# Optimization experiments

Measured on AMD Instinct MI355X. Metric: run time of the kernel, lower is better.

The kernel has to match this reference:

```python
import jax, jax.numpy as jnp
import numpy as np

N_NODES = 100000
N_EDGES = 1000000
N_QUERY = 100000
F_IN = 64
HIDDEN = 64
LABEL_DIM = 2


def setup_inputs() -> dict:
    key = jax.random.key(0)
    ks = jax.random.split(key, 16)
    inp = {}
    for i, nm in enumerate(["Xr", "Xi", "Xj", "Xk"]):
        inp[nm] = jax.random.normal(ks[i], (N_NODES, F_IN), dtype=jnp.float32)
    for i, nm in enumerate(["norm_r", "norm_i", "norm_j", "norm_k"]):
        inp[nm] = jax.random.normal(ks[4 + i], (N_EDGES,), dtype=jnp.float32) * 0.1
    inp["edge_index"] = jax.random.randint(ks[8], (2, N_EDGES), 0, N_NODES)
    inp["query_edges"] = jax.random.randint(ks[9], (N_QUERY, 2), 0, N_NODES)
    s1 = (2.0 / (F_IN + HIDDEN)) ** 0.5  # glorot
    inp["W1"] = jax.random.normal(ks[10], (4, F_IN, HIDDEN), dtype=jnp.float32) * s1
    inp["b1"] = jnp.zeros((4, HIDDEN), dtype=jnp.float32)
    s2 = (2.0 / (HIDDEN + HIDDEN)) ** 0.5
    inp["W2"] = jax.random.normal(ks[11], (4, HIDDEN, HIDDEN), dtype=jnp.float32) * s2
    inp["b2"] = jnp.zeros((4, HIDDEN), dtype=jnp.float32)
    inp["Cw"] = jax.random.normal(ks[12], (LABEL_DIM, 8 * HIDDEN), dtype=jnp.float32) * 0.05
    inp["Cb"] = jnp.zeros((LABEL_DIM,), dtype=jnp.float32)
    return inp


def _quaconv(Xs, src, dst, norms, W, b, n_nodes):
    # Xs: list of 4 [N,F] components; norms: list of 4 [E] Laplacian norms.
    # P[a][b] = propagate(X_a, -norm_b) = scatter_add over dst of (-norm_b)_e * X_a[src_e]
    P = []
    for a in range(4):
        G = Xs[a][src]  # [E, F] gather, reused for all 4 norms
        P.append([jax.ops.segment_sum((-norms[b])[:, None] * G, dst, num_segments=n_nodes)
                  for b in range(4)])
    Tr = P[0][0] - P[1][1] - P[2][2] - P[3][3]
    Ti = P[1][0] + P[0][1] + P[3][2] - P[2][3]
    Tj = P[2][0] - P[3][1] + P[0][2] + P[1][3]
    Tk = P[3][0] + P[2][1] - P[1][2] + P[0][3]
    Wr, Wi, Wj, Wk = W[0], W[1], W[2], W[3]
    out_r = Tr @ Wr - Ti @ Wi - Tj @ Wj - Tk @ Wk + b[0]
    out_i = Tr @ Wi + Ti @ Wr + Tj @ Wk - Tk @ Wj + b[1]
    out_j = Tr @ Wj - Ti @ Wk + Tj @ Wr + Tk @ Wi + b[2]
    out_k = Tr @ Wk + Ti @ Wj - Tj @ Wi + Tk @ Wr + b[3]
    return out_r, out_i, out_j, out_k


def _forward(Xr, Xi, Xj, Xk, norm_r, norm_i, norm_j, norm_k,
             W1, b1, W2, b2, Cw, Cb, edge_index, query_edges):
    src, dst = edge_index[0], edge_index[1]
    n = Xr.shape[0]
    norms = [norm_r, norm_i, norm_j, norm_k]
    Xs = [Xr, Xi, Xj, Xk]
    for W, b in ((W1, b1), (W2, b2)):
        Xs = list(_quaconv(Xs, src, dst, norms, W, b, n))
        # complex_relu_layer_different: mask = 1.0*(x>=0); mask*x == relu(x)
        Xs = [jax.nn.relu(x) for x in Xs]
    q0, q1 = query_edges[:, 0], query_edges[:, 1]
    # cat(real[q0], real[q1], imag_i[q0], imag_i[q1], ...) -> [Eq, 8*hidden]
    feats = jnp.concatenate([c[idx] for c in Xs for idx in (q0, q1)], axis=-1)
    # dropout is identity at inference; Conv1d(kernel=1) == linear over channels
    logits = feats @ Cw.T + Cb  # [Eq, label_dim]
    return jax.nn.log_softmax(logits, axis=-1)


def reference(Xr, Xi, Xj, Xk, norm_r, norm_i, norm_j, norm_k,
              W1, b1, W2, b2, Cw, Cb, edge_index, query_edges):
    return _forward(Xr, Xi, Xj, Xk, norm_r, norm_i, norm_j, norm_k,
                    W1, b1, W2, b2, Cw, Cb, edge_index, query_edges)
```

## Files before the change

kernel.cpp:

```cpp
#include <hip/hip_runtime.h>
#include <hip/hip_bf16.h>

#define N_NODESC 100000
#define N_EDGESC 1000000
#define N_QUERYC 100000

typedef short short8 __attribute__((ext_vector_type(8)));
typedef short s16x2 __attribute__((ext_vector_type(2)));
typedef float f32x4 __attribute__((ext_vector_type(4)));

__device__ __forceinline__ float ldf(const void* p, int i, int isbf) {
  return isbf ? __bfloat162float(((const __hip_bfloat16*)p)[i])
              : ((const float*)p)[i];
}
__device__ __forceinline__ unsigned short f2b(float x) {
  __hip_bfloat16 h = __float2bfloat16(x);
  return *(unsigned short*)&h;
}
__device__ __forceinline__ float b2f(unsigned int u) {
  return __uint_as_float(u << 16);
}
__device__ __forceinline__ s16x2 u2s(unsigned u) {
  union { unsigned u; s16x2 s; } c; c.u = u; return c.s;
}
__device__ __forceinline__ void gload16(const void* g, void* l) {
  __builtin_amdgcn_global_load_lds(
      (const __attribute__((address_space(1))) void*)g,
      (__attribute__((address_space(3))) void*)l, 16, 0, 0);
}

__global__ void k_sniff(const void* x, int* flag) {
  __shared__ int cnt;
  int t = threadIdx.x;
  if (t == 0) cnt = 0;
  __syncthreads();
  const unsigned short* h = (const unsigned short*)x;
  int local = 0;
  for (int i = t; i < 4096; i += 256) {
    int e = (h[i] >> 7) & 0xFF;
    if (e >= 107 && e <= 133) local++;
  }
  atomicAdd(&cnt, local);
  __syncthreads();
  if (t == 0) *flag = (cnt >= 3482) ? 1 : 0;
}

__global__ void k_hist(const int* __restrict__ dst, int* __restrict__ cnt, int ne) {
  int e = blockIdx.x * 256 + threadIdx.x;
  if (e < ne) atomicAdd(&cnt[dst[e]], 1);
}

__global__ void k_scan1(const int* __restrict__ cnt, int* __restrict__ off,
                        int* __restrict__ partials, int n) {
  __shared__ int s[1024];
  int t = threadIdx.x;
  int idx = blockIdx.x * 1024 + t;
  int v = (idx < n) ? cnt[idx] : 0;
  s[t] = v;
  __syncthreads();
  for (int d = 1; d < 1024; d <<= 1) {
    int tmp = (t >= d) ? s[t - d] : 0;
    __syncthreads();
    s[t] += tmp;
    __syncthreads();
  }
  if (idx < n) off[idx] = s[t] - v;
  if (t == 1023) partials[blockIdx.x] = s[1023];
}

__global__ void k_scan2(const int* __restrict__ partials, int* __restrict__ pref,
                        int* __restrict__ off, int nb, int npos) {
  __shared__ int s[128];
  int t = threadIdx.x;
  int v = (t < nb) ? partials[t] : 0;
  s[t] = v;
  __syncthreads();
  for (int d = 1; d < 128; d <<= 1) {
    int tmp = (t >= d) ? s[t - d] : 0;
    __syncthreads();
    s[t] += tmp;
    __syncthreads();
  }
  if (t < nb) pref[t] = s[t] - v;
  if (t == 127) off[npos] = s[127];
}

__global__ void k_scan3(int* __restrict__ off, const int* __restrict__ pref,
                        int* __restrict__ cursor, int n) {
  int i = blockIdx.x * 256 + threadIdx.x;
  if (i < n) {
    int o = off[i] + pref[i >> 10];
    off[i] = o;
    cursor[i] = o;
  }
}

__global__ void k_fill(const int* __restrict__ ei,
                       const void* nr, const void* ni, const void* nj, const void* nk,
                       const int* __restrict__ flagp, int* __restrict__ cursor,
                       uint4* __restrict__ recs, int ne) {
  int isbf = *flagp;
  int e = blockIdx.x * 256 + threadIdx.x;
  if (e >= ne) return;
  int s = ei[e];
  int d = ei[ne + e];
  int pos = atomicAdd(&cursor[d], 1);
  uint4 r;
  r.x = (unsigned)s;
  r.y = (unsigned)f2b(-ldf(nr, e, isbf)) | ((unsigned)f2b(-ldf(ni, e, isbf)) << 16);
  r.z = (unsigned)f2b(-ldf(nj, e, isbf)) | ((unsigned)f2b(-ldf(nk, e, isbf)) << 16);
  r.w = 0;
  recs[pos] = r;
}

__global__ __launch_bounds__(256) void k_ilv(
    const void* X0, const void* X1, const void* X2, const void* X3,
    const int* __restrict__ flagp, unsigned short* __restrict__ Xg, int n) {
  int isbf = *flagp;
  int lane = threadIdx.x & 63;
  int node = blockIdx.x * 4 + (threadIdx.x >> 6);
  if (node >= n) return;
  int idx = node * 64 + lane;
  unsigned int lo = f2b(ldf(X0, idx, isbf)) | ((unsigned int)f2b(ldf(X1, idx, isbf)) << 16);
  unsigned int hi = f2b(ldf(X2, idx, isbf)) | ((unsigned int)f2b(ldf(X3, idx, isbf)) << 16);
  uint2 g = make_uint2(lo, hi);
  *(uint2*)(Xg + (size_t)node * 256 + lane * 4) = g;
}

#if __has_builtin(__builtin_amdgcn_fdot2_f32_bf16)
#define USE_DOT2 1
#else
#define USE_DOT2 0
#endif
__global__ __launch_bounds__(256, 8) void k_agg(
    const unsigned short* __restrict__ Xg, const int* __restrict__ off,
    const uint4* __restrict__ recs, unsigned short* __restrict__ Tf, int nnodes) {
  __shared__ unsigned short tl[4][256];
  int lane = threadIdx.x & 63;
  int w = threadIdx.x >> 6;
  int node = __builtin_amdgcn_readfirstlane(blockIdx.x * 4 + w);
  if (node >= nnodes) return;
  int rs = off[node], re = off[node + 1];
  float tr = 0.f, ti = 0.f, tj = 0.f, tk = 0.f;

  auto qacc = [&](uint2 g, unsigned mx, unsigned my) {
#if USE_DOT2
    unsigned a = mx, b = my;
    unsigned sa = (a >> 16) | (a << 16);
    unsigned sb = (b >> 16) | (b << 16);
    unsigned A1 = a ^ 0x80000000u;
    unsigned A2 = b ^ 0x80008000u;
    unsigned B2 = sb ^ 0x00008000u;
    unsigned D2 = sb ^ 0x80000000u;
    s16x2 gx = u2s(g.x), gy = u2s(g.y);
    tr = __builtin_amdgcn_fdot2_f32_bf16(u2s(A1), gx, tr, false);
    tr = __builtin_amdgcn_fdot2_f32_bf16(u2s(A2), gy, tr, false);
    ti = __builtin_amdgcn_fdot2_f32_bf16(u2s(sa), gx, ti, false);
    ti = __builtin_amdgcn_fdot2_f32_bf16(u2s(B2), gy, ti, false);
    tj = __builtin_amdgcn_fdot2_f32_bf16(u2s(b),  gx, tj, false);
    tj = __builtin_amdgcn_fdot2_f32_bf16(u2s(A1), gy, tj, false);
    tk = __builtin_amdgcn_fdot2_f32_bf16(u2s(D2), gx, tk, false);
    tk = __builtin_amdgcn_fdot2_f32_bf16(u2s(sa), gy, tk, false);
#else
    float mr = __uint_as_float(mx << 16), mi = __uint_as_float(mx & 0xffff0000u);
    float mj = __uint_as_float(my << 16), mk = __uint_as_float(my & 0xffff0000u);
    float xr = __uint_as_float(g.x << 16), xi = __uint_as_float(g.x & 0xffff0000u);
    float xj = __uint_as_float(g.y << 16), xk = __uint_as_float(g.y & 0xffff0000u);
    tr += mr * xr - mi * xi - mj * xj - mk * xk;
    ti += mr * xi + mi * xr + mj * xk - mk * xj;
    tj += mr * xj - mi * xk + mj * xr + mk * xi;
    tk += mr * xk + mi * xj - mj * xi + mk * xr;
#endif
  };

  int e = rs;
  for (; e + 8 <= re; e += 8) {
    int ss[8];
    unsigned sx[8], sy[8];
#pragma unroll
    for (int u = 0; u < 8; u++) {
      uint4 r = recs[e + u];
      ss[u] = __builtin_amdgcn_readfirstlane((int)r.x);
      sx[u] = __builtin_amdgcn_readfirstlane(r.y);
      sy[u] = __builtin_amdgcn_readfirstlane(r.z);
    }
    uint2 g[8];
#pragma unroll
    for (int u = 0; u < 8; u++)
      g[u] = *(const uint2*)(Xg + (size_t)ss[u] * 256 + lane * 4);
#pragma unroll
    for (int u = 0; u < 8; u++) qacc(g[u], sx[u], sy[u]);
  }
  for (; e < re; ++e) {
    uint4 r = recs[e];
    int s = __builtin_amdgcn_readfirstlane((int)r.x);
    unsigned mx = __builtin_amdgcn_readfirstlane(r.y);
    unsigned my = __builtin_amdgcn_readfirstlane(r.z);
    uint2 g0 = *(const uint2*)(Xg + (size_t)s * 256 + lane * 4);
    qacc(g0, mx, my);
  }

  tl[w][lane] = f2b(tr);
  tl[w][64 + lane] = f2b(ti);
  tl[w][128 + lane] = f2b(tj);
  tl[w][192 + lane] = f2b(tk);
  __builtin_amdgcn_wave_barrier();
  if (lane < 32) {
    uint4 v = *(const uint4*)&tl[w][lane * 8];
    size_t o = (size_t)(node >> 4) * 4096 + (lane >> 2) * 512 + (lane & 3) * 128 +
               (node & 15) * 8;
    *(uint4*)(Tf + o) = v;
  }
}

__global__ void k_weff(const void* W, const void* b, const int* __restrict__ flagp,
                       unsigned short* __restrict__ Wq, float* __restrict__ bcat) {
  int isbf = *flagp;
  int t = blockIdx.x * 256 + threadIdx.x;
  int w4 = t >> 12;
  int h = (t >> 6) & 63;
  int kk = t & 63;
  int s = (kk >> 3) ^ (h & 7);
  Wq[(w4 * 64 + h) * 64 + s * 8 + (kk & 7)] = f2b(ldf(W, w4 * 4096 + kk * 64 + h, isbf));
  if (t < 256) bcat[t] = ldf(b, t, isbf);
}

__global__ __launch_bounds__(256, 2) void k_gemm(
    const unsigned short* __restrict__ A, const unsigned short* __restrict__ Wq,
    const float* __restrict__ bias, int M, int mode,
    unsigned short* __restrict__ XgOut,
    float* __restrict__ P, const void* Cw, const int* __restrict__ flagp) {
  __shared__ unsigned short Wsm[16384];

  int t = threadIdx.x;
  int lane = t & 63;
  int w = t >> 6;
  int l15 = lane & 15, quad = lane >> 4;
  int m0 = blockIdx.x * 64;
  int hh = (w & 1) * 32;

#pragma unroll
  for (int i = 0; i < 8; i++)
    gload16((const char*)Wq + (size_t)(i * 256 + t) * 16,
            (char*)Wsm + (size_t)(i * 256 + w * 64) * 16);
  __syncthreads();

  short8 av[2][8];
  int n16 = blockIdx.x * 4 + (w >> 1) * 2;
#pragma unroll
  for (int mi = 0; mi < 2; mi++)
#pragma unroll
    for (int kc = 0; kc < 8; kc++)
      av[mi][kc] = *(const short8*)(A + (size_t)(n16 + mi) * 4096 + kc * 512 + lane * 8);

  f32x4 acc[2][4][2];
#pragma unroll
  for (int mi = 0; mi < 2; mi++)
#pragma unroll
    for (int c = 0; c < 4; c++)
#pragma unroll
      for (int hb = 0; hb < 2; hb++) acc[mi][c][hb] = (f32x4){0.f, 0.f, 0.f, 0.f};

#pragma unroll
  for (int kc = 0; kc < 8; kc++) {
    int a = kc >> 1;
    short8 bv[4][2];
#pragma unroll
    for (int c = 0; c < 4; c++) {
      int w4 = a ^ c;
      int neg = (0x3950 >> (a * 4 + c)) & 1;
#pragma unroll
      for (int hb = 0; hb < 2; hb++) {
        int h = hh + hb * 16 + l15;
        int lc = ((kc & 1) * 4 + quad) ^ (l15 & 7);
        short8 bb = *(const short8*)&Wsm[(w4 * 64 + h) * 64 + lc * 8];
        if (neg) {
          uint4 u = *(uint4*)&bb;
          u.x ^= 0x80008000u; u.y ^= 0x80008000u;
          u.z ^= 0x80008000u; u.w ^= 0x80008000u;
          bb = *(short8*)&u;
        }
        bv[c][hb] = bb;
      }
    }
#pragma unroll
    for (int mi = 0; mi < 2; mi++)
#pragma unroll
      for (int c = 0; c < 4; c++)
#pragma unroll
        for (int hb = 0; hb < 2; hb++)
          acc[mi][c][hb] =
              __builtin_amdgcn_mfma_f32_16x16x32_bf16(av[mi][kc], bv[c][hb], acc[mi][c][hb], 0, 0, 0);
  }

  float bias_v[4][2];
#pragma unroll
  for (int c = 0; c < 4; c++)
#pragma unroll
    for (int hb = 0; hb < 2; hb++) bias_v[c][hb] = bias[c * 64 + hh + hb * 16 + l15];

  if (mode == 0) {
#pragma unroll
    for (int mi = 0; mi < 2; mi++) {
#pragma unroll
      for (int hb = 0; hb < 2; hb++) {
#pragma unroll
        for (int r = 0; r < 4; r++) {
          int node = m0 + (w >> 1) * 32 + mi * 16 + quad * 4 + r;
          unsigned int lo =
              f2b(fmaxf(acc[mi][0][hb][r] + bias_v[0][hb], 0.f)) |
              ((unsigned int)f2b(fmaxf(acc[mi][1][hb][r] + bias_v[1][hb], 0.f)) << 16);
          unsigned int hi =
              f2b(fmaxf(acc[mi][2][hb][r] + bias_v[2][hb], 0.f)) |
              ((unsigned int)f2b(fmaxf(acc[mi][3][hb][r] + bias_v[3][hb], 0.f)) << 16);
          *(uint2*)(XgOut + (size_t)node * 256 + (hh + hb * 16 + l15) * 4) =
              make_uint2(lo, hi);
        }
      }
    }
  } else {
    int isbf = *flagp;
    float cw[4][2][4];
#pragma unroll
    for (int c = 0; c < 4; c++)
#pragma unroll
      for (int hb = 0; hb < 2; hb++) {
        int h = hh + hb * 16 + l15;
#pragma unroll
        for (int d = 0; d < 2; d++)
#pragma unroll
          for (int e = 0; e < 2; e++)
            cw[c][hb][e + 2 * d] = ldf(Cw, d * 512 + c * 128 + e * 64 + h, isbf);
      }
#pragma unroll
    for (int mi = 0; mi < 2; mi++) {
#pragma unroll
      for (int r = 0; r < 4; r++) {
        int node = m0 + (w >> 1) * 32 + mi * 16 + quad * 4 + r;
        float pd0 = 0.f, pd1 = 0.f, pd2 = 0.f, pd3 = 0.f;
#pragma unroll
        for (int c = 0; c < 4; c++)
#pragma unroll
          for (int hb = 0; hb < 2; hb++) {
            float v = fmaxf(acc[mi][c][hb][r] + bias_v[c][hb], 0.f);
            pd0 += v * cw[c][hb][0];
            pd1 += v * cw[c][hb][1];
            pd2 += v * cw[c][hb][2];
            pd3 += v * cw[c][hb][3];
          }
#pragma unroll
        for (int o = 1; o < 16; o <<= 1) {
          pd0 += __shfl_xor(pd0, o);
          pd1 += __shfl_xor(pd1, o);
          pd2 += __shfl_xor(pd2, o);
          pd3 += __shfl_xor(pd3, o);
        }
        if (l15 == 0 && node < M) {
          atomicAdd(&P[node * 4 + 0], pd0);
          atomicAdd(&P[node * 4 + 1], pd1);
          atomicAdd(&P[node * 4 + 2], pd2);
          atomicAdd(&P[node * 4 + 3], pd3);
        }
      }
    }
  }
}

__global__ void k_query(const int* __restrict__ qe, const float* __restrict__ P,
                        const void* Cb, const int* __restrict__ flagp,
                        void* out, int nq) {
  int isbf = *flagp;
  int q = blockIdx.x * 256 + threadIdx.x;
  if (q >= nq) return;
  int q0 = qe[q * 2], q1 = qe[q * 2 + 1];
  float l0 = P[q0 * 4 + 0] + P[q1 * 4 + 1] + ldf(Cb, 0, isbf);
  float l1 = P[q0 * 4 + 2] + P[q1 * 4 + 3] + ldf(Cb, 1, isbf);
  float m = fmaxf(l0, l1);
  float lse = m + logf(expf(l0 - m) + expf(l1 - m));
  float o0 = l0 - lse, o1 = l1 - lse;
  if (isbf) {
    __hip_bfloat16* o = (__hip_bfloat16*)out;
    o[q * 2] = __float2bfloat16(o0);
    o[q * 2 + 1] = __float2bfloat16(o1);
  } else {
    float* o = (float*)out;
    o[q * 2] = o0;
    o[q * 2 + 1] = o1;
  }
}

extern "C" void kernel_launch(void* const* d_in, const int* in_sizes, int n_in,
                              void* d_out, int out_size, void* d_ws, size_t ws_size,
                              hipStream_t stream) {
  const int N = N_NODESC, NE = N_EDGESC, NQ = N_QUERYC;
  const int NPAD = 100224;

  char* w = (char*)d_ws;
  auto alloc = [&](size_t bytes) -> void* {
    void* p = (void*)w;
    w += (bytes + 255) & ~(size_t)255;
    return p;
  };
  int* flag       = (int*)alloc(4);
  int* offsets    = (int*)alloc((size_t)(N + 1) * 4);
  int* cursor     = (int*)alloc((size_t)N * 4);
  int* partials   = (int*)alloc(128 * 4);
  int* pref       = (int*)alloc(128 * 4);
  uint4* recs     = (uint4*)alloc((size_t)NE * 16);
  unsigned short* Tf = (unsigned short*)alloc((size_t)NPAD * 256 * 2);
  unsigned short* Xg = (unsigned short*)alloc((size_t)NPAD * 256 * 2);
  unsigned short* Wq = (unsigned short*)alloc(16384 * 2);
  float* bcat     = (float*)alloc(256 * 4);
  float* P        = (float*)alloc((size_t)N * 4 * 4);
  (void)ws_size; (void)n_in; (void)in_sizes; (void)out_size;

  const int* ei = (const int*)d_in[8];

  k_sniff<<<1, 256, 0, stream>>>(d_in[0], flag);

  hipMemsetAsync(cursor, 0, (size_t)N * 4, stream);
  hipMemsetAsync(P, 0, (size_t)N * 16, stream);
  k_hist<<<(NE + 255) / 256, 256, 0, stream>>>(ei + NE, cursor, NE);
  k_scan1<<<(N + 1023) / 1024, 1024, 0, stream>>>(cursor, offsets, partials, N);
  k_scan2<<<1, 128, 0, stream>>>(partials, pref, offsets, (N + 1023) / 1024, N);
  k_scan3<<<(N + 255) / 256, 256, 0, stream>>>(offsets, pref, cursor, N);
  k_fill<<<(NE + 255) / 256, 256, 0, stream>>>(ei, d_in[4], d_in[5], d_in[6], d_in[7],
                                               flag, cursor, recs, NE);

  k_ilv<<<(N + 3) / 4, 256, 0, stream>>>(d_in[0], d_in[1], d_in[2], d_in[3], flag, Xg, N);

  int ggrid = (N + 63) / 64;

  k_agg<<<(N + 3) / 4, 256, 0, stream>>>(Xg, offsets, recs, Tf, N);
  k_weff<<<64, 256, 0, stream>>>(d_in[10], d_in[11], flag, Wq, bcat);
  k_gemm<<<ggrid, 256, 0, stream>>>(Tf, Wq, bcat, N, 0, Xg, nullptr, nullptr, flag);

  k_agg<<<(N + 3) / 4, 256, 0, stream>>>(Xg, offsets, recs, Tf, N);
  k_weff<<<64, 256, 0, stream>>>(d_in[12], d_in[13], flag, Wq, bcat);
  k_gemm<<<ggrid, 256, 0, stream>>>(Tf, Wq, bcat, N, 1, nullptr, P, d_in[14], flag);

  k_query<<<(NQ + 255) / 256, 256, 0, stream>>>((const int*)d_in[9], P, d_in[15],
                                                flag, d_out, NQ);
}
```

Measured before the change: 553.5 us.

## Balance aggregation by edges per wave with software-pipelined record and gather loads

Result: slower. 613.0 us (+10.8%).

```diff
diff --git a/kernel.cpp b/kernel.cpp
--- a/kernel.cpp
+++ b/kernel.cpp
@@ -4,6 +4,7 @@
 #define N_NODESC 100000
 #define N_EDGESC 1000000
 #define N_QUERYC 100000
+#define AGG_WAVES 8192
 
 typedef short short8 __attribute__((ext_vector_type(8)));
 typedef short s16x2 __attribute__((ext_vector_type(2)));
@@ -93,6 +94,20 @@
     off[i] = o;
     cursor[i] = o;
   }
+}
+
+__global__ void k_bounds(const int* __restrict__ off, int* __restrict__ bound,
+                         int nnodes, int nedges, int nwaves) {
+  int gw = blockIdx.x * 256 + threadIdx.x;
+  if (gw > nwaves) return;
+  if (gw == nwaves) { bound[gw] = nnodes; return; }
+  long long target = (long long)gw * nedges / nwaves;
+  int lo = 0, hi = nnodes;
+  while (lo < hi) {
+    int mid = (lo + hi) >> 1;
+    if ((long long)off[mid] >= target) hi = mid; else lo = mid + 1;
+  }
+  bound[gw] = lo;
 }
 
 __global__ void k_fill(const int* __restrict__ ei,
@@ -132,16 +147,43 @@
 #else
 #define USE_DOT2 0
 #endif
-__global__ __launch_bounds__(256, 8) void k_agg(
+__global__ __launch_bounds__(256, 4) void k_agg(
     const unsigned short* __restrict__ Xg, const int* __restrict__ off,
-    const uint4* __restrict__ recs, unsigned short* __restrict__ Tf, int nnodes) {
+    const uint4* __restrict__ recs, unsigned short* __restrict__ Tf,
+    const int* __restrict__ bound, int nnodes, int nwaves) {
   __shared__ unsigned short tl[4][256];
   int lane = threadIdx.x & 63;
   int w = threadIdx.x >> 6;
-  int node = __builtin_amdgcn_readfirstlane(blockIdx.x * 4 + w);
-  if (node >= nnodes) return;
-  int rs = off[node], re = off[node + 1];
+  int gw = blockIdx.x * 4 + w;
+  if (gw >= nwaves) return;
+
+  int ns  = __builtin_amdgcn_readfirstlane(bound[gw]);
+  int ne_ = __builtin_amdgcn_readfirstlane(bound[gw + 1]);
+  if (ns >= ne_) return;
+  int es = __builtin_amdgcn_readfirstlane(off[ns]);
+  int ee = __builtin_amdgcn_readfirstlane(off[ne_]);
+
+  int nw_ = ns;
+  int rend_e = __builtin_amdgcn_readfirstlane(off[nw_ + 1]);
   float tr = 0.f, ti = 0.f, tj = 0.f, tk = 0.f;
+
+  auto flush = [&]() {
+    tl[w][lane] = f2b(tr);
+    tl[w][64 + lane] = f2b(ti);
+    tl[w][128 + lane] = f2b(tj);
+    tl[w][192 + lane] = f2b(tk);
+    __builtin_amdgcn_wave_barrier();
+    if (lane < 32) {
+      uint4 v = *(const uint4*)&tl[w][lane * 8];
+      size_t o = (size_t)(nw_ >> 4) * 4096 + (lane >> 2) * 512 + (lane & 3) * 128 +
+                 (nw_ & 15) * 8;
+      *(uint4*)(Tf + o) = v;
+    }
+    __builtin_amdgcn_wave_barrier();
+    tr = ti = tj = tk = 0.f;
+    nw_++;
+    if (nw_ < ne_) rend_e = __builtin_amdgcn_readfirstlane(off[nw_ + 1]);
+  };
 
   auto qacc = [&](uint2 g, unsigned mx, unsigned my) {
 #if USE_DOT2
@@ -173,44 +215,97 @@
 #endif
   };
 
-  int e = rs;
-  for (; e + 8 <= re; e += 8) {
-    int ss[8];
-    unsigned sx[8], sy[8];
-#pragma unroll
-    for (int u = 0; u < 8; u++) {
-      uint4 r = recs[e + u];
-      ss[u] = __builtin_amdgcn_readfirstlane((int)r.x);
-      sx[u] = __builtin_amdgcn_readfirstlane(r.y);
-      sy[u] = __builtin_amdgcn_readfirstlane(r.z);
-    }
-    uint2 g[8];
-#pragma unroll
-    for (int u = 0; u < 8; u++)
-      g[u] = *(const uint2*)(Xg + (size_t)ss[u] * 256 + lane * 4);
-#pragma unroll
-    for (int u = 0; u < 8; u++) qacc(g[u], sx[u], sy[u]);
-  }
-  for (; e < re; ++e) {
-    uint4 r = recs[e];
+  uint4 rA[4], rB[4];
+  int ssA[4], ssB[4];
+  unsigned sxA[4], syA[4], sxB[4], syB[4];
+  uint2 gA[4], gB[4];
+
+  auto RLOAD_A = [&](int base) {
+#pragma unroll
+    for (int u = 0; u < 4; u++) rA[u] = recs[base + u];
+  };
+  auto RLOAD_B = [&](int base) {
+#pragma unroll
+    for (int u = 0; u < 4; u++) rB[u] = recs[base + u];
+  };
+  auto RFL_A = [&]() {
+#pragma unroll
+    for (int u = 0; u < 4; u++) {
+      ssA[u] = __builtin_amdgcn_readfirstlane((int)rA[u].x);
+      sxA[u] = __builtin_amdgcn_readfirstlane(rA[u].y);
+      syA[u] = __builtin_amdgcn_readfirstlane(rA[u].z);
+    }
+  };
+  auto RFL_B = [&]() {
+#pragma unroll
+    for (int u = 0; u < 4; u++) {
+      ssB[u] = __builtin_amdgcn_readfirstlane((int)rB[u].x);
+      sxB[u] = __builtin_amdgcn_readfirstlane(rB[u].y);
+      syB[u] = __builtin_amdgcn_readfirstlane(rB[u].z);
+    }
+  };
+  auto GATH_A = [&]() {
+#pragma unroll
+    for (int u = 0; u < 4; u++)
+      gA[u] = *(const uint2*)(Xg + (size_t)ssA[u] * 256 + lane * 4);
+  };
+  auto GATH_B = [&]() {
+#pragma unroll
+    for (int u = 0; u < 4; u++)
+      gB[u] = *(const uint2*)(Xg + (size_t)ssB[u] * 256 + lane * 4);
+  };
+  auto COMP_A = [&](int base) {
+#pragma unroll
+    for (int u = 0; u < 4; u++) {
+      int eg = base + u;
+      while (eg == rend_e) flush();
+      qacc(gA[u], sxA[u], syA[u]);
+    }
+  };
+  auto COMP_B = [&](int base) {
+#pragma unroll
+    for (int u = 0; u < 4; u++) {
+      int eg = base + u;
+      while (eg == rend_e) flush();
+      qacc(gB[u], sxB[u], syB[u]);
+    }
+  };
+
+  int len = ee - es;
+  int nc = len >> 2;
+  int rem = len & 3;
+
+  if (nc >= 1) {
+    RLOAD_A(es);
+    RFL_A();
+    if (nc >= 2) RLOAD_B(es + 4);
+    GATH_A();
+    if (nc >= 2) RFL_B();
+    for (int c = 0; c < nc; c += 2) {
+      if (c + 2 < nc) RLOAD_A(es + (c + 2) * 4);
+      if (c + 1 < nc) GATH_B();
+      COMP_A(es + c * 4);
+      if (c + 2 < nc) RFL_A();
+      if (c + 1 >= nc) break;
+      if (c + 3 < nc) RLOAD_B(es + (c + 3) * 4);
+      if (c + 2 < nc) GATH_A();
+      COMP_B(es + (c + 1) * 4);
+      if (c + 3 < nc) RFL_B();
+    }
+  }
+
+  for (int q = 0; q < rem; ++q) {
+    int eg = es + nc * 4 + q;
+    uint4 r = recs[eg];
     int s = __builtin_amdgcn_readfirstlane((int)r.x);
     unsigned mx = __builtin_amdgcn_readfirstlane(r.y);
     unsigned my = __builtin_amdgcn_readfirstlane(r.z);
     uint2 g0 = *(const uint2*)(Xg + (size_t)s * 256 + lane * 4);
+    while (eg == rend_e) flush();
     qacc(g0, mx, my);
   }
 
-  tl[w][lane] = f2b(tr);
-  tl[w][64 + lane] = f2b(ti);
-  tl[w][128 + lane] = f2b(tj);
-  tl[w][192 + lane] = f2b(tk);
-  __builtin_amdgcn_wave_barrier();
-  if (lane < 32) {
-    uint4 v = *(const uint4*)&tl[w][lane * 8];
-    size_t o = (size_t)(node >> 4) * 4096 + (lane >> 2) * 512 + (lane & 3) * 128 +
-               (node & 15) * 8;
-    *(uint4*)(Tf + o) = v;
-  }
+  while (nw_ < ne_) flush();
 }
 
 __global__ void k_weff(const void* W, const void* b, const int* __restrict__ flagp,
@@ -394,6 +489,7 @@
                               hipStream_t stream) {
   const int N = N_NODESC, NE = N_EDGESC, NQ = N_QUERYC;
   const int NPAD = 100224;
+  const int NW = AGG_WAVES;
 
   char* w = (char*)d_ws;
   auto alloc = [&](size_t bytes) -> void* {
@@ -406,6 +502,7 @@
   int* cursor     = (int*)alloc((size_t)N * 4);
   int* partials   = (int*)alloc(128 * 4);
   int* pref       = (int*)alloc(128 * 4);
+  int* bound      = (int*)alloc((size_t)(NW + 1) * 4);
   uint4* recs     = (uint4*)alloc((size_t)NE * 16);
   unsigned short* Tf = (unsigned short*)alloc((size_t)NPAD * 256 * 2);
   unsigned short* Xg = (unsigned short*)alloc((size_t)NPAD * 256 * 2);
@@ -424,6 +521,7 @@
   k_scan1<<<(N + 1023) / 1024, 1024, 0, stream>>>(cursor, offsets, partials, N);
   k_scan2<<<1, 128, 0, stream>>>(partials, pref, offsets, (N + 1023) / 1024, N);
   k_scan3<<<(N + 255) / 256, 256, 0, stream>>>(offsets, pref, cursor, N);
+  k_bounds<<<(NW + 256) / 256, 256, 0, stream>>>(offsets, bound, N, NE, NW);
   k_fill<<<(NE + 255) / 256, 256, 0, stream>>>(ei, d_in[4], d_in[5], d_in[6], d_in[7],
                                                flag, cursor, recs, NE);
 
@@ -431,11 +529,11 @@
 
   int ggrid = (N + 63) / 64;
 
-  k_agg<<<(N + 3) / 4, 256, 0, stream>>>(Xg, offsets, recs, Tf, N);
+  k_agg<<<NW / 4, 256, 0, stream>>>(Xg, offsets, recs, Tf, bound, N, NW);
   k_weff<<<64, 256, 0, stream>>>(d_in[10], d_in[11], flag, Wq, bcat);
   k_gemm<<<ggrid, 256, 0, stream>>>(Tf, Wq, bcat, N, 0, Xg, nullptr, nullptr, flag);
 
-  k_agg<<<(N + 3) / 4, 256, 0, stream>>>(Xg, offsets, recs, Tf, N);
+  k_agg<<<NW / 4, 256, 0, stream>>>(Xg, offsets, recs, Tf, bound, N, NW);
   k_weff<<<64, 256, 0, stream>>>(d_in[12], d_in[13], flag, Wq, bcat);
   k_gemm<<<ggrid, 256, 0, stream>>>(Tf, Wq, bcat, N, 1, nullptr, P, d_in[14], flag);
 
```

## Balance aggregation by edges: each wave processes a contiguous node range

Applied to the files above, without the earlier changes.

Result: slower. 611.0 us (+10.4%).

```diff
diff --git a/kernel.cpp b/kernel.cpp
--- a/kernel.cpp
+++ b/kernel.cpp
@@ -4,6 +4,7 @@
 #define N_NODESC 100000
 #define N_EDGESC 1000000
 #define N_QUERYC 100000
+#define AGG_WAVES 8192
 
 typedef short short8 __attribute__((ext_vector_type(8)));
 typedef short s16x2 __attribute__((ext_vector_type(2)));
@@ -93,6 +94,20 @@
     off[i] = o;
     cursor[i] = o;
   }
+}
+
+__global__ void k_bounds(const int* __restrict__ off, int* __restrict__ bound,
+                         int nnodes, int nedges, int nwaves) {
+  int gw = blockIdx.x * 256 + threadIdx.x;
+  if (gw > nwaves) return;
+  if (gw == nwaves) { bound[gw] = nnodes; return; }
+  long long target = (long long)gw * nedges / nwaves;
+  int lo = 0, hi = nnodes;
+  while (lo < hi) {
+    int mid = (lo + hi) >> 1;
+    if ((long long)off[mid] >= target) hi = mid; else lo = mid + 1;
+  }
+  bound[gw] = lo;
 }
 
 __global__ void k_fill(const int* __restrict__ ei,
@@ -134,14 +149,41 @@
 #endif
 __global__ __launch_bounds__(256, 8) void k_agg(
     const unsigned short* __restrict__ Xg, const int* __restrict__ off,
-    const uint4* __restrict__ recs, unsigned short* __restrict__ Tf, int nnodes) {
+    const uint4* __restrict__ recs, unsigned short* __restrict__ Tf,
+    const int* __restrict__ bound, int nnodes, int nwaves) {
   __shared__ unsigned short tl[4][256];
   int lane = threadIdx.x & 63;
   int w = threadIdx.x >> 6;
-  int node = __builtin_amdgcn_readfirstlane(blockIdx.x * 4 + w);
-  if (node >= nnodes) return;
-  int rs = off[node], re = off[node + 1];
+  int gw = blockIdx.x * 4 + w;
+  if (gw >= nwaves) return;
+
+  int ns  = __builtin_amdgcn_readfirstlane(bound[gw]);
+  int ne_ = __builtin_amdgcn_readfirstlane(bound[gw + 1]);
+  if (ns >= ne_) return;
+  int es = __builtin_amdgcn_readfirstlane(off[ns]);
+  int ee = __builtin_amdgcn_readfirstlane(off[ne_]);
+
+  int nw_ = ns;
+  int rend_e = __builtin_amdgcn_readfirstlane(off[nw_ + 1]);
   float tr = 0.f, ti = 0.f, tj = 0.f, tk = 0.f;
+
+  auto flush = [&]() {
+    tl[w][lane] = f2b(tr);
+    tl[w][64 + lane] = f2b(ti);
+    tl[w][128 + lane] = f2b(tj);
+    tl[w][192 + lane] = f2b(tk);
+    __builtin_amdgcn_wave_barrier();
+    if (lane < 32) {
+      uint4 v = *(const uint4*)&tl[w][lane * 8];
+      size_t o = (size_t)(nw_ >> 4) * 4096 + (lane >> 2) * 512 + (lane & 3) * 128 +
+                 (nw_ & 15) * 8;
+      *(uint4*)(Tf + o) = v;
+    }
+    __builtin_amdgcn_wave_barrier();
+    tr = ti = tj = tk = 0.f;
+    nw_++;
+    if (nw_ < ne_) rend_e = __builtin_amdgcn_readfirstlane(off[nw_ + 1]);
+  };
 
   auto qacc = [&](uint2 g, unsigned mx, unsigned my) {
 #if USE_DOT2
@@ -173,44 +215,47 @@
 #endif
   };
 
-  int e = rs;
-  for (; e + 8 <= re; e += 8) {
+  int len = ee - es;
+  int nc = len >> 3;
+  int rem = len & 7;
+
+  for (int c = 0; c < nc; ++c) {
+    int base = es + c * 8;
+    uint4 r[8];
+#pragma unroll
+    for (int u = 0; u < 8; u++) r[u] = recs[base + u];
     int ss[8];
     unsigned sx[8], sy[8];
 #pragma unroll
     for (int u = 0; u < 8; u++) {
-      uint4 r = recs[e + u];
-      ss[u] = __builtin_amdgcn_readfirstlane((int)r.x);
-      sx[u] = __builtin_amdgcn_readfirstlane(r.y);
-      sy[u] = __builtin_amdgcn_readfirstlane(r.z);
+      ss[u] = __builtin_amdgcn_readfirstlane((int)r[u].x);
+      sx[u] = __builtin_amdgcn_readfirstlane(r[u].y);
+      sy[u] = __builtin_amdgcn_readfirstlane(r[u].z);
     }
     uint2 g[8];
 #pragma unroll
     for (int u = 0; u < 8; u++)
       g[u] = *(const uint2*)(Xg + (size_t)ss[u] * 256 + lane * 4);
 #pragma unroll
-    for (int u = 0; u < 8; u++) qacc(g[u], sx[u], sy[u]);
-  }
-  for (; e < re; ++e) {
-    uint4 r = recs[e];
+    for (int u = 0; u < 8; u++) {
+      int eg = base + u;
+      while (eg == rend_e) flush();
+      qacc(g[u], sx[u], sy[u]);
+    }
+  }
+
+  for (int q = 0; q < rem; ++q) {
+    int eg = es + nc * 8 + q;
+    uint4 r = recs[eg];
     int s = __builtin_amdgcn_readfirstlane((int)r.x);
     unsigned mx = __builtin_amdgcn_readfirstlane(r.y);
     unsigned my = __builtin_amdgcn_readfirstlane(r.z);
     uint2 g0 = *(const uint2*)(Xg + (size_t)s * 256 + lane * 4);
+    while (eg == rend_e) flush();
     qacc(g0, mx, my);
   }
 
-  tl[w][lane] = f2b(tr);
-  tl[w][64 + lane] = f2b(ti);
-  tl[w][128 + lane] = f2b(tj);
-  tl[w][192 + lane] = f2b(tk);
-  __builtin_amdgcn_wave_barrier();
-  if (lane < 32) {
-    uint4 v = *(const uint4*)&tl[w][lane * 8];
-    size_t o = (size_t)(node >> 4) * 4096 + (lane >> 2) * 512 + (lane & 3) * 128 +
-               (node & 15) * 8;
-    *(uint4*)(Tf + o) = v;
-  }
+  while (nw_ < ne_) flush();
 }
 
 __global__ void k_weff(const void* W, const void* b, const int* __restrict__ flagp,
@@ -394,6 +439,7 @@
                               hipStream_t stream) {
   const int N = N_NODESC, NE = N_EDGESC, NQ = N_QUERYC;
   const int NPAD = 100224;
+  const int NW = AGG_WAVES;
 
   char* w = (char*)d_ws;
   auto alloc = [&](size_t bytes) -> void* {
@@ -406,6 +452,7 @@
   int* cursor     = (int*)alloc((size_t)N * 4);
   int* partials   = (int*)alloc(128 * 4);
   int* pref       = (int*)alloc(128 * 4);
+  int* bound      = (int*)alloc((size_t)(NW + 1) * 4);
   uint4* recs     = (uint4*)alloc((size_t)NE * 16);
   unsigned short* Tf = (unsigned short*)alloc((size_t)NPAD * 256 * 2);
   unsigned short* Xg = (unsigned short*)alloc((size_t)NPAD * 256 * 2);
@@ -424,6 +471,7 @@
   k_scan1<<<(N + 1023) / 1024, 1024, 0, stream>>>(cursor, offsets, partials, N);
   k_scan2<<<1, 128, 0, stream>>>(partials, pref, offsets, (N + 1023) / 1024, N);
   k_scan3<<<(N + 255) / 256, 256, 0, stream>>>(offsets, pref, cursor, N);
+  k_bounds<<<(NW + 256) / 256, 256, 0, stream>>>(offsets, bound, N, NE, NW);
   k_fill<<<(NE + 255) / 256, 256, 0, stream>>>(ei, d_in[4], d_in[5], d_in[6], d_in[7],
                                                flag, cursor, recs, NE);
 
@@ -431,11 +479,11 @@
 
   int ggrid = (N + 63) / 64;
 
-  k_agg<<<(N + 3) / 4, 256, 0, stream>>>(Xg, offsets, recs, Tf, N);
+  k_agg<<<NW / 4, 256, 0, stream>>>(Xg, offsets, recs, Tf, bound, N, NW);
   k_weff<<<64, 256, 0, stream>>>(d_in[10], d_in[11], flag, Wq, bcat);
   k_gemm<<<ggrid, 256, 0, stream>>>(Tf, Wq, bcat, N, 0, Xg, nullptr, nullptr, flag);
 
-  k_agg<<<(N + 3) / 4, 256, 0, stream>>>(Xg, offsets, recs, Tf, N);
+  k_agg<<<NW / 4, 256, 0, stream>>>(Xg, offsets, recs, Tf, bound, N, NW);
   k_weff<<<64, 256, 0, stream>>>(d_in[12], d_in[13], flag, Wq, bcat);
   k_gemm<<<ggrid, 256, 0, stream>>>(Tf, Wq, bcat, N, 1, nullptr, P, d_in[14], flag);
 
```
